# Optimization experiments

Measured on AMD Instinct MI355X. Metric: run time of the kernel, lower is better.

## Reference

```python
import jax, jax.numpy as jnp
import numpy as np

NEG_SLOPE = 0.2
EPS = 1e-12


def setup_inputs() -> dict:
    key = jax.random.key(0)
    ks = jax.random.split(key, 12)
    N, IN, E, C, EF, NET = 100000, 512, 3200000, 16, 64, 8
    return {
        "head_feature": jax.random.normal(ks[0], (N, IN), jnp.float32),
        "tail_feature": jax.random.normal(ks[1], (N, IN), jnp.float32),
        "edge_index": jax.random.randint(ks[2], (2, E), 0, N, jnp.int32),
        "tmp_edge": jax.random.randint(ks[3], (E,), 0, NET, jnp.int32),
        "W": jax.random.normal(ks[4], (IN, C), jnp.float32) * 0.05,
        "W_e": jax.random.normal(ks[5], (EF, EF), jnp.float32) * 0.1,
        "a_l": jax.random.normal(ks[6], (1, 1, C), jnp.float32) * 0.3,
        "a_r": jax.random.normal(ks[7], (1, 1, C), jnp.float32) * 0.3,
        "a_e": jax.random.normal(ks[8], (1, 1, EF), jnp.float32) * 0.3,
        "edge_emb": jax.random.normal(ks[9], (NET, EF), jnp.float32) * 0.3,
        "res_W": jax.random.normal(ks[10], (IN, C), jnp.float32) * 0.05,
        "res_b": jax.random.normal(ks[11], (C,), jnp.float32) * 0.05,
    }


def reference(head_feature, tail_feature, W, W_e, a_l, a_r, a_e,
              edge_emb, res_W, res_b, edge_index, tmp_edge):
    N = head_feature.shape[0]
    H = a_l.shape[1]  # nhead = 1 in SimpleHGN_final's edge_GAT
    C = a_l.shape[2]
    head_ind, tail_ind = edge_index[0], edge_index[1]

    # projected node / edge-type features (dropout is identity in eval)
    h_head = (head_feature @ W).reshape(N, H, C)              # [N,H,C]
    h_tail = (tail_feature @ W).reshape(-1, H, C)             # [Nt,H,C]
    e = (edge_emb @ W_e).reshape(-1, H, a_e.shape[2])         # [NET,H,EF]

    # per-edge attention logits
    h_l = (a_l * h_head).sum(-1)[head_ind]                    # [E,H]
    h_r = (a_r * h_tail).sum(-1)[tail_ind]                    # [E,H]
    h_e = (a_e * e).sum(-1)[tmp_edge]                         # [E,H]
    logits = jax.nn.leaky_relu(h_l + h_r + h_e, NEG_SLOPE)    # [E,H]

    # sparse softmax over each destination (head) row, per head
    m = jax.ops.segment_max(logits, head_ind, num_segments=N)  # [N,H]
    ex = jnp.exp(logits - m[head_ind])
    denom = jax.ops.segment_sum(ex, head_ind, num_segments=N)  # [N,H]
    attn = ex / denom[head_ind]                                # [E,H]

    # SpMM aggregation: out[i] = sum_e attn[e] * h_tail[tail[e]]
    msg = attn[..., None] * h_tail[tail_ind]                   # [E,H,C]
    out = jax.ops.segment_sum(msg, head_ind, num_segments=N)   # [N,H,C]
    out = out.reshape(N, H * C)

    # node residual (nn.Linear on x_head)
    out = out + head_feature @ res_W + res_b

    # SimpleHGN_final post-processing: L2 row-normalize then softmax
    norm = jnp.linalg.norm(out, axis=1, keepdims=True)
    h_prime = out / jnp.maximum(norm, EPS)
    return jax.nn.softmax(h_prime, axis=1)
```

## Files before the change

### kernel.cpp

```cpp
#include <hip/hip_runtime.h>
#include <hip/hip_fp16.h>
#include <math.h>

#define IN_F 512
#define C_DIM 16
#define EF_DIM 64
#define BSHIFT 6
#define NPB 64
#define NBMAX2 2048
#define CNTW 2048
#define SCB 512
#define NSPL 8
#define CAP 2560

typedef float f32x4 __attribute__((ext_vector_type(4)));
typedef _Float16 f16x8 __attribute__((ext_vector_type(8)));

union U2H { unsigned u; __half2 h; };

typedef const unsigned __attribute__((address_space(1)))* gas_u32;
typedef unsigned __attribute__((address_space(3)))* las_u32;

__device__ __forceinline__ void gld16(const float* g, float* l) {
  __builtin_amdgcn_global_load_lds((gas_u32)g, (las_u32)l, 16, 0, 0);
}

__global__ __launch_bounds__(512) void prep_kernel(
    const float* __restrict__ W, const float* __restrict__ We,
    const float* __restrict__ al, const float* __restrict__ ar,
    const float* __restrict__ ae, const float* __restrict__ emb,
    const float* __restrict__ resW, float* __restrict__ he,
    _Float16* __restrict__ Bph, _Float16* __restrict__ Bpt,
    float* __restrict__ wlt, float* __restrict__ wrt, int NET) {
  __shared__ float v[EF_DIM];
  int t = threadIdx.x;
  float wl = 0.f, wr = 0.f;
#pragma unroll
  for (int c = 0; c < C_DIM; c++) {
    float wv = W[t * C_DIM + c];
    wl += wv * al[c];
    wr += wv * ar[c];
  }
  wlt[t] = wl;
  wrt[t] = wr;
  if (t < EF_DIM) {
    float s = 0.f;
    for (int f = 0; f < EF_DIM; f++) s += We[t * EF_DIM + f] * ae[f];
    v[t] = s;
  }
  __syncthreads();
  if (t < NET) {
    float s = 0.f;
    for (int k = 0; k < EF_DIM; k++) s += emb[t * EF_DIM + k] * v[k];
    he[t] = s;
  }
  for (int i = 0; i < 16; i++) {
    int flat = t + 512 * i;
    int j = flat & 7;
    int l = (flat >> 3) & 63;
    int s = flat >> 9;
    int k = 32 * s + ((l >> 4) << 3) + j;
    int c = l & 15;
    Bph[flat] = (_Float16)resW[k * C_DIM + c];
    Bpt[flat] = (_Float16)W[k * C_DIM + c];
  }
}

__global__ __launch_bounds__(256) void projhist_kernel(
    const float* __restrict__ hf, const float* __restrict__ tf,
    const _Float16* __restrict__ Bph, const _Float16* __restrict__ Bpt,
    const float* __restrict__ wlt, const float* __restrict__ wrt,
    float* __restrict__ resid, float* __restrict__ hl,
    __half* __restrict__ ht_, float* __restrict__ hr, int N, int PB,
    const int* __restrict__ head, unsigned* __restrict__ cnt, int E, int NB,
    int chunk) {
  __shared__ __align__(16) float shmem[8192];
  int t = threadIdx.x;
  int bid = blockIdx.x;
  if (bid >= 2 * PB) {
    unsigned* lcnt = (unsigned*)shmem;
    int hb = bid - 2 * PB;
    for (int b = t; b < NB; b += 256) lcnt[b] = 0u;
    __syncthreads();
    int start = hb * chunk;
    int end = min(E, start + chunk);
    for (int i = start + t; i < end; i += 256)
      atomicAdd(
          &lcnt[((unsigned)__builtin_nontemporal_load(head + i)) >> BSHIFT],
          1u);
    __syncthreads();
    unsigned* row = cnt + (size_t)hb * CNTW;
    for (int b = t; b < NB; b += 256) row[b] = lcnt[b];
    return;
  }
  float* As0 = shmem;
  float* As1 = shmem + 4096;
  int w = __builtin_amdgcn_readfirstlane(t >> 6);
  int lane = t & 63;
  int by = bid >= PB ? 1 : 0;
  int r0 = (bid - by * PB) * 64;
  const float* feat = by ? tf : hf;
  const _Float16* Bp = by ? Bpt : Bph;
  const float* wv = by ? wrt : wlt;
  f32x4 acc0 = {0.f, 0.f, 0.f, 0.f};
  float acc1 = 0.f;
  const float* sg_src[4];
#pragma unroll
  for (int g = 0; g < 4; g++) {
    int u = (w * 4 + g) * 64 + lane;
    int r = u >> 4;
    int c = (u & 15) ^ (r & 7);
    int gr = min(r0 + r, N - 1);
    sg_src[g] = feat + (size_t)gr * IN_F + c * 4;
  }
  int row = w * 16 + (lane & 15);
  int sA[2][2];
#pragma unroll
  for (int s2 = 0; s2 < 2; s2++)
#pragma unroll
    for (int h = 0; h < 2; h++)
      sA[s2][h] = row * 16 + ((s2 * 8 + (lane >> 4) * 2 + h) ^ (row & 7));
  const float* wvp = wv + (lane >> 4) * 8;
#pragma unroll
  for (int g = 0; g < 4; g++) gld16(sg_src[g], As0 + (w * 4 + g) * 256);
  __syncthreads();
#pragma unroll
  for (int kc = 0; kc < 8; kc++) {
    if (kc < 7) {
      float* nb = (kc & 1) ? As0 : As1;
#pragma unroll
      for (int g = 0; g < 4; g++)
        gld16(sg_src[g] + (kc + 1) * 64, nb + (w * 4 + g) * 256);
    }
    const float* ab = (kc & 1) ? As1 : As0;
#pragma unroll
    for (int s2 = 0; s2 < 2; s2++) {
      f32x4 lo = *(const f32x4*)(ab + sA[s2][0] * 4);
      f32x4 hi = *(const f32x4*)(ab + sA[s2][1] * 4);
      f16x8 a = {(_Float16)lo.x, (_Float16)lo.y, (_Float16)lo.z,
                 (_Float16)lo.w, (_Float16)hi.x, (_Float16)hi.y,
                 (_Float16)hi.z, (_Float16)hi.w};
      int s = kc * 2 + s2;
      f16x8 b0 = *(const f16x8*)(Bp + (size_t)(s * 64 + lane) * 8);
      acc0 = __builtin_amdgcn_mfma_f32_16x16x32_f16(a, b0, acc0, 0, 0, 0);
      f32x4 wa = *(const f32x4*)(wvp + kc * 64 + s2 * 32);
      f32x4 wb = *(const f32x4*)(wvp + kc * 64 + s2 * 32 + 4);
      acc1 += lo.x * wa.x + lo.y * wa.y + lo.z * wa.z + lo.w * wa.w +
              hi.x * wb.x + hi.y * wb.y + hi.z * wb.z + hi.w * wb.w;
    }
    __syncthreads();
  }
  acc1 += __shfl_xor(acc1, 16, 64);
  acc1 += __shfl_xor(acc1, 32, 64);
  int col = lane & 15;
  int rb = r0 + w * 16 + (lane >> 4) * 4;
#pragma unroll
  for (int i = 0; i < 4; i++) {
    int r = rb + i;
    if (r < N) {
      if (by == 0)
        resid[(size_t)r * C_DIM + col] = acc0[i];
      else
        ht_[(size_t)r * C_DIM + col] = __float2half(acc0[i]);
    }
  }
  if (lane < 16) {
    int r = r0 + w * 16 + lane;
    if (r < N) {
      if (by == 0)
        hl[r] = acc1;
      else
        hr[r] = acc1;
    }
  }
}

__global__ __launch_bounds__(256) void colscanA_kernel(
    unsigned* __restrict__ cnt, unsigned* __restrict__ part, int NB) {
  int b = blockIdx.x * 256 + threadIdx.x;
  if (b >= NB) return;
  int s = blockIdx.y;
  unsigned running = 0;
#pragma unroll 8
  for (int blk = s * 64; blk < s * 64 + 64; blk++) {
    unsigned v = cnt[(size_t)blk * CNTW + b];
    cnt[(size_t)blk * CNTW + b] = running;
    running += v;
  }
  part[(size_t)s * CNTW + b] = running;
}

__global__ __launch_bounds__(256) void colscanB_kernel(
    unsigned* __restrict__ part, unsigned* __restrict__ btotal, int NB) {
  int b = blockIdx.x * 256 + threadIdx.x;
  if (b >= NB) return;
  unsigned running = 0;
#pragma unroll
  for (int s = 0; s < NSPL; s++) {
    unsigned v = part[(size_t)s * CNTW + b];
    part[(size_t)s * CNTW + b] = running;
    running += v;
  }
  btotal[b] = running;
}

__global__ __launch_bounds__(1024) void scan_kernel(
    const unsigned* __restrict__ btotal, unsigned* __restrict__ base, int NB) {
  __shared__ unsigned ps[1024];
  int t = threadIdx.x;
  unsigned a = (2 * t < NB) ? btotal[2 * t] : 0u;
  unsigned b = (2 * t + 1 < NB) ? btotal[2 * t + 1] : 0u;
  ps[t] = a + b;
  __syncthreads();
  for (int off = 1; off < 1024; off <<= 1) {
    unsigned v = (t >= off) ? ps[t - off] : 0u;
    __syncthreads();
    ps[t] += v;
    __syncthreads();
  }
  unsigned excl = ps[t] - (a + b);
  if (2 * t < NB) base[2 * t] = excl;
  if (2 * t + 1 < NB) base[2 * t + 1] = excl + a;
  if (t == 1023) base[NB] = ps[1023];
}

__global__ __launch_bounds__(512) void scatter_kernel(
    const int* __restrict__ head, const int* __restrict__ tail,
    const int* __restrict__ ty, const unsigned* __restrict__ cnt,
    const unsigned* __restrict__ part, const unsigned* __restrict__ bbase,
    unsigned* __restrict__ rec, int E, int NB, int chunk) {
  __shared__ unsigned lbase[NBMAX2];
  __shared__ unsigned lcnt[NBMAX2];
  int tid = threadIdx.x;
  int blk = blockIdx.x;
  const unsigned* row = cnt + (size_t)blk * CNTW;
  const unsigned* prow = part + (size_t)(blk >> 6) * CNTW;
  for (int b = tid; b < NB; b += 512) {
    lbase[b] = bbase[b] + prow[b] + row[b];
    lcnt[b] = 0u;
  }
  __syncthreads();
  int start = blk * chunk;
  int end = min(E, start + chunk);
  for (int i = start + tid; i < end; i += 512) {
    unsigned h = (unsigned)__builtin_nontemporal_load(head + i);
    unsigned tl = (unsigned)__builtin_nontemporal_load(tail + i);
    unsigned t = (unsigned)__builtin_nontemporal_load(ty + i);
    unsigned b = h >> BSHIFT;
    unsigned off = atomicAdd(&lcnt[b], 1u);
    rec[lbase[b] + off] = ((h & 63u) << 20) | ((t & 7u) << 17) | tl;
  }
}

__global__ __launch_bounds__(512) void agg_kernel(
    const unsigned* __restrict__ rec, const unsigned* __restrict__ base,
    const __half* __restrict__ ht, const float* __restrict__ h_l,
    const float* __restrict__ h_r, const float* __restrict__ he_tab,
    const float* __restrict__ resid, const float* __restrict__ resb,
    float* __restrict__ out, int N, int NET) {
  __shared__ unsigned srec[CAP];
  __shared__ unsigned scnt[NPB];
  __shared__ unsigned soff[NPB + 1];
  __shared__ unsigned scur[NPB];
  __shared__ float accf[NPB * 18];
  __shared__ float hl_s[NPB];
  __shared__ float he_s[8];
  int tid = threadIdx.x;
  int b = blockIdx.x;
  int nodebase = b << BSHIFT;
  int s = (int)base[b];
  int e = (int)base[b + 1];
  int cnt_all = e - s;
  int m = min(cnt_all, CAP);
  if (tid < NPB) {
    scnt[tid] = 0u;
    int node = nodebase + tid;
    hl_s[tid] = node < N ? h_l[node] : 0.f;
  }
  if (tid < NET) he_s[tid] = he_tab[tid];
  for (int i = tid; i < NPB * 18; i += 512) accf[i] = 0.f;
  __syncthreads();
  unsigned rv0 = 0, rv1 = 0, rv2 = 0, rv3 = 0, rv4 = 0;
  if (tid < m) rv0 = rec[(size_t)s + tid];
  if (tid + 512 < m) rv1 = rec[(size_t)s + tid + 512];
  if (tid + 1024 < m) rv2 = rec[(size_t)s + tid + 1024];
  if (tid + 1536 < m) rv3 = rec[(size_t)s + tid + 1536];
  if (tid + 2048 < m) rv4 = rec[(size_t)s + tid + 2048];
  if (tid < m) atomicAdd(&scnt[rv0 >> 20], 1u);
  if (tid + 512 < m) atomicAdd(&scnt[rv1 >> 20], 1u);
  if (tid + 1024 < m) atomicAdd(&scnt[rv2 >> 20], 1u);
  if (tid + 1536 < m) atomicAdd(&scnt[rv3 >> 20], 1u);
  if (tid + 2048 < m) atomicAdd(&scnt[rv4 >> 20], 1u);
  __syncthreads();
  if (tid < NPB) {
    unsigned v = scnt[tid];
    unsigned orig = v;
    for (int off = 1; off < NPB; off <<= 1) {
      unsigned u = __shfl_up(v, off, 64);
      if (tid >= off) v += u;
    }
    soff[tid + 1] = v;
    scur[tid] = v - orig;
    if (tid == 0) soff[0] = 0u;
  }
  __syncthreads();
  if (tid < m) srec[atomicAdd(&scur[rv0 >> 20], 1u)] = rv0;
  if (tid + 512 < m) srec[atomicAdd(&scur[rv1 >> 20], 1u)] = rv1;
  if (tid + 1024 < m) srec[atomicAdd(&scur[rv2 >> 20], 1u)] = rv2;
  if (tid + 1536 < m) srec[atomicAdd(&scur[rv3 >> 20], 1u)] = rv3;
  if (tid + 2048 < m) srec[atomicAdd(&scur[rv4 >> 20], 1u)] = rv4;
  for (int i = CAP + tid; i < cnt_all; i += 512) {
    unsigned r = rec[(size_t)(s + i)];
    int local = (int)(r >> 20);
    int typ = (int)((r >> 17) & 7u);
    int tl = (int)(r & 0x1FFFFu);
    float lg = hl_s[local] + h_r[tl] + he_s[typ];
    lg = lg > 0.f ? lg : 0.2f * lg;
    float ex = __expf(lg);
    const uint4* hp = (const uint4*)(ht + (size_t)tl * C_DIM);
    uint4 A = hp[0], B = hp[1];
    float* a = accf + local * 18;
    U2H cv;
    float2 f;
    unsigned wvv[8] = {A.x, A.y, A.z, A.w, B.x, B.y, B.z, B.w};
#pragma unroll
    for (int q = 0; q < 8; q++) {
      cv.u = wvv[q];
      f = __half22float2(cv.h);
      atomicAdd(a + 2 * q, ex * f.x);
      atomicAdd(a + 2 * q + 1, ex * f.y);
    }
    atomicAdd(a + 16, ex);
  }
  __syncthreads();
  int w = tid >> 6;
  int lane = tid & 63;
  int node_l = w * 8 + (lane >> 3);
  int p = lane & 7;
  float a[17];
#pragma unroll
  for (int k = 0; k < 17; k++) a[k] = 0.f;
  int st = (int)soff[node_l];
  int en = (int)soff[node_l + 1];
  float hlv = hl_s[node_l];
  for (int i = st + p; i < en; i += 8) {
    unsigned r = srec[i];
    int typ = (int)((r >> 17) & 7u);
    int tl = (int)(r & 0x1FFFFu);
    float lg = hlv + h_r[tl] + he_s[typ];
    lg = lg > 0.f ? lg : 0.2f * lg;
    float ex = __expf(lg);
    const uint4* hp = (const uint4*)(ht + (size_t)tl * C_DIM);
    uint4 A = hp[0], B = hp[1];
    U2H cv;
    float2 f;
    unsigned wd[8] = {A.x, A.y, A.z, A.w, B.x, B.y, B.z, B.w};
#pragma unroll
    for (int q = 0; q < 8; q++) {
      cv.u = wd[q];
      f = __half22float2(cv.h);
      a[2 * q] += ex * f.x;
      a[2 * q + 1] += ex * f.y;
    }
    a[16] += ex;
  }
#pragma unroll
  for (int k = 0; k < 17; k++) {
    a[k] += __shfl_xor(a[k], 1, 64);
    a[k] += __shfl_xor(a[k], 2, 64);
    a[k] += __shfl_xor(a[k], 4, 64);
  }
  if (p != 0) return;
  int node = nodebase + node_l;
  if (node >= N) return;
  float d = a[16] + accf[node_l * 18 + 16];
  float inv = d > 0.f ? 1.f / d : 0.f;
  const f32x4* r4 = (const f32x4*)(resid + (size_t)node * C_DIM);
  float o[C_DIM];
  float ss = 0.f;
#pragma unroll
  for (int q = 0; q < 4; q++) {
    f32x4 rr = __builtin_nontemporal_load(r4 + q);
    o[4 * q + 0] =
        (a[4 * q + 0] + accf[node_l * 18 + 4 * q + 0]) * inv + rr.x + resb[4 * q + 0];
    o[4 * q + 1] =
        (a[4 * q + 1] + accf[node_l * 18 + 4 * q + 1]) * inv + rr.y + resb[4 * q + 1];
    o[4 * q + 2] =
        (a[4 * q + 2] + accf[node_l * 18 + 4 * q + 2]) * inv + rr.z + resb[4 * q + 2];
    o[4 * q + 3] =
        (a[4 * q + 3] + accf[node_l * 18 + 4 * q + 3]) * inv + rr.w + resb[4 * q + 3];
  }
#pragma unroll
  for (int cc = 0; cc < C_DIM; cc++) ss += o[cc] * o[cc];
  float sc = 1.f / fmaxf(sqrtf(ss), 1e-12f);
  float mx = -1e30f;
#pragma unroll
  for (int cc = 0; cc < C_DIM; cc++) {
    o[cc] *= sc;
    mx = fmaxf(mx, o[cc]);
  }
  float sum = 0.f;
#pragma unroll
  for (int cc = 0; cc < C_DIM; cc++) {
    o[cc] = __expf(o[cc] - mx);
    sum += o[cc];
  }
  float isum = 1.f / sum;
  f32x4* o4 = (f32x4*)(out + (size_t)node * C_DIM);
#pragma unroll
  for (int q = 0; q < 4; q++) {
    f32x4 ov;
    ov.x = o[4 * q] * isum;
    ov.y = o[4 * q + 1] * isum;
    ov.z = o[4 * q + 2] * isum;
    ov.w = o[4 * q + 3] * isum;
    __builtin_nontemporal_store(ov, o4 + q);
  }
}

extern "C" void kernel_launch(void* const* d_in, const int* in_sizes, int n_in,
                              void* d_out, int out_size, void* d_ws,
                              size_t ws_size, hipStream_t stream) {
  const float* head_feature = (const float*)d_in[0];
  const float* tail_feature = (const float*)d_in[1];
  const int* edge_index = (const int*)d_in[2];
  const int* tmp_edge = (const int*)d_in[3];
  const float* W = (const float*)d_in[4];
  const float* We = (const float*)d_in[5];
  const float* al = (const float*)d_in[6];
  const float* ar = (const float*)d_in[7];
  const float* ae = (const float*)d_in[8];
  const float* emb = (const float*)d_in[9];
  const float* resW = (const float*)d_in[10];
  const float* resb = (const float*)d_in[11];

  const int C = in_sizes[6];
  const int IN = in_sizes[4] / C;
  const int N = in_sizes[0] / IN;
  const int E = in_sizes[3];
  const int EF = in_sizes[8];
  const int NET = in_sizes[9] / EF;
  const int NB = (N + NPB - 1) / NPB;
  (void)C; (void)IN; (void)EF; (void)ws_size; (void)out_size; (void)n_in;

  const int* head = edge_index;
  const int* tail = edge_index + E;

  float* ws = (float*)d_ws;
  float* he = ws;
  _Float16* Bph = (_Float16*)(he + 32);
  _Float16* Bpt = Bph + 8192;
  float* wlt = (float*)(Bpt + 8192);
  float* wrt = wlt + 512;
  float* h_l = wrt + 512;
  float* h_r = h_l + N;
  __half* ht = (__half*)(h_r + N);
  float* resid = (float*)(ht + (size_t)C_DIM * N);
  unsigned* rec = (unsigned*)(resid + (size_t)C_DIM * N);
  unsigned* cnt = rec + (size_t)E;
  unsigned* part = cnt + (size_t)SCB * CNTW;
  unsigned* btotal = part + (size_t)NSPL * CNTW;
  unsigned* bbase = btotal + NBMAX2;

  prep_kernel<<<1, 512, 0, stream>>>(W, We, al, ar, ae, emb, resW, he, Bph,
                                     Bpt, wlt, wrt, NET);
  int PB = (N + 63) / 64;
  int chunk = (E + SCB - 1) / SCB;
  projhist_kernel<<<2 * PB + SCB, 256, 0, stream>>>(
      head_feature, tail_feature, Bph, Bpt, wlt, wrt, resid, h_l, ht, h_r, N,
      PB, head, cnt, E, NB, chunk);
  dim3 cg((NB + 255) / 256, NSPL);
  colscanA_kernel<<<cg, 256, 0, stream>>>(cnt, part, NB);
  colscanB_kernel<<<(NB + 255) / 256, 256, 0, stream>>>(part, btotal, NB);
  scan_kernel<<<1, 1024, 0, stream>>>(btotal, bbase, NB);
  scatter_kernel<<<SCB, 512, 0, stream>>>(head, tail, tmp_edge, cnt, part,
                                          bbase, rec, E, NB, chunk);
  agg_kernel<<<NB, 512, 0, stream>>>(rec, bbase, ht, h_l, h_r, he, resid,
                                     resb, (float*)d_out, N, NET);
}
```

Measured before the change: 225.2 us.

## Regroup kernels: fuse histogram into prep, scatter into projection

Moves the per-block head histogram into the single-block prep kernel launch, and merges the edge scatter pass with the node projection GEMM kernel, which now runs after the scans. This removes one kernel launch and lets the memory-bound scatter overlap with the compute-heavier projection blocks. The trade-off is that the histogram no longer overlaps the projection, and the scatter now runs with 256-thread blocks instead of 512.

Result: faster. 201.3 us (-10.6%).

```diff
diff --git a/kernel.cpp b/kernel.cpp
--- a/kernel.cpp
+++ b/kernel.cpp
@@ -25,15 +25,33 @@
   __builtin_amdgcn_global_load_lds((gas_u32)g, (las_u32)l, 16, 0, 0);
 }
 
-__global__ __launch_bounds__(512) void prep_kernel(
+__global__ __launch_bounds__(512) void prephist_kernel(
     const float* __restrict__ W, const float* __restrict__ We,
     const float* __restrict__ al, const float* __restrict__ ar,
     const float* __restrict__ ae, const float* __restrict__ emb,
     const float* __restrict__ resW, float* __restrict__ he,
     _Float16* __restrict__ Bph, _Float16* __restrict__ Bpt,
-    float* __restrict__ wlt, float* __restrict__ wrt, int NET) {
+    float* __restrict__ wlt, float* __restrict__ wrt, int NET,
+    const int* __restrict__ head, unsigned* __restrict__ cnt, int E, int NB,
+    int chunk) {
+  __shared__ unsigned lcnt[NBMAX2];
   __shared__ float v[EF_DIM];
   int t = threadIdx.x;
+  int bid = blockIdx.x;
+  if (bid < SCB) {
+    for (int b = t; b < NB; b += 512) lcnt[b] = 0u;
+    __syncthreads();
+    int start = bid * chunk;
+    int end = min(E, start + chunk);
+    for (int i = start + t; i < end; i += 512)
+      atomicAdd(
+          &lcnt[((unsigned)__builtin_nontemporal_load(head + i)) >> BSHIFT],
+          1u);
+    __syncthreads();
+    unsigned* row = cnt + (size_t)bid * CNTW;
+    for (int b = t; b < NB; b += 512) row[b] = lcnt[b];
+    return;
+  }
   float wl = 0.f, wr = 0.f;
 #pragma unroll
   for (int c = 0; c < C_DIM; c++) {
@@ -66,39 +84,48 @@
   }
 }
 
-__global__ __launch_bounds__(256) void projhist_kernel(
+__global__ __launch_bounds__(256) void projscatter_kernel(
     const float* __restrict__ hf, const float* __restrict__ tf,
     const _Float16* __restrict__ Bph, const _Float16* __restrict__ Bpt,
     const float* __restrict__ wlt, const float* __restrict__ wrt,
     float* __restrict__ resid, float* __restrict__ hl,
     __half* __restrict__ ht_, float* __restrict__ hr, int N, int PB,
-    const int* __restrict__ head, unsigned* __restrict__ cnt, int E, int NB,
-    int chunk) {
+    const int* __restrict__ head, const int* __restrict__ tail,
+    const int* __restrict__ ty, const unsigned* __restrict__ cnt,
+    const unsigned* __restrict__ part, const unsigned* __restrict__ bbase,
+    unsigned* __restrict__ rec, int E, int NB, int chunk) {
   __shared__ __align__(16) float shmem[8192];
   int t = threadIdx.x;
   int bid = blockIdx.x;
-  if (bid >= 2 * PB) {
-    unsigned* lcnt = (unsigned*)shmem;
-    int hb = bid - 2 * PB;
-    for (int b = t; b < NB; b += 256) lcnt[b] = 0u;
-    __syncthreads();
-    int start = hb * chunk;
+  if (bid < SCB) {
+    unsigned* lbase = (unsigned*)shmem;
+    unsigned* lcnt = lbase + NBMAX2;
+    const unsigned* row = cnt + (size_t)bid * CNTW;
+    const unsigned* prow = part + (size_t)(bid >> 6) * CNTW;
+    for (int b = t; b < NB; b += 256) {
+      lbase[b] = bbase[b] + prow[b] + row[b];
+      lcnt[b] = 0u;
+    }
+    __syncthreads();
+    int start = bid * chunk;
     int end = min(E, start + chunk);
-    for (int i = start + t; i < end; i += 256)
-      atomicAdd(
-          &lcnt[((unsigned)__builtin_nontemporal_load(head + i)) >> BSHIFT],
-          1u);
-    __syncthreads();
-    unsigned* row = cnt + (size_t)hb * CNTW;
-    for (int b = t; b < NB; b += 256) row[b] = lcnt[b];
+    for (int i = start + t; i < end; i += 256) {
+      unsigned h = (unsigned)__builtin_nontemporal_load(head + i);
+      unsigned tl = (unsigned)__builtin_nontemporal_load(tail + i);
+      unsigned tt = (unsigned)__builtin_nontemporal_load(ty + i);
+      unsigned b = h >> BSHIFT;
+      unsigned off = atomicAdd(&lcnt[b], 1u);
+      rec[lbase[b] + off] = ((h & 63u) << 20) | ((tt & 7u) << 17) | tl;
+    }
     return;
   }
   float* As0 = shmem;
   float* As1 = shmem + 4096;
   int w = __builtin_amdgcn_readfirstlane(t >> 6);
   int lane = t & 63;
-  int by = bid >= PB ? 1 : 0;
-  int r0 = (bid - by * PB) * 64;
+  int pbid = bid - SCB;
+  int by = pbid >= PB ? 1 : 0;
+  int r0 = (pbid - by * PB) * 64;
   const float* feat = by ? tf : hf;
   const _Float16* Bp = by ? Bpt : Bph;
   const float* wv = by ? wrt : wlt;
@@ -222,34 +249,6 @@
   if (2 * t < NB) base[2 * t] = excl;
   if (2 * t + 1 < NB) base[2 * t + 1] = excl + a;
   if (t == 1023) base[NB] = ps[1023];
-}
-
-__global__ __launch_bounds__(512) void scatter_kernel(
-    const int* __restrict__ head, const int* __restrict__ tail,
-    const int* __restrict__ ty, const unsigned* __restrict__ cnt,
-    const unsigned* __restrict__ part, const unsigned* __restrict__ bbase,
-    unsigned* __restrict__ rec, int E, int NB, int chunk) {
-  __shared__ unsigned lbase[NBMAX2];
-  __shared__ unsigned lcnt[NBMAX2];
-  int tid = threadIdx.x;
-  int blk = blockIdx.x;
-  const unsigned* row = cnt + (size_t)blk * CNTW;
-  const unsigned* prow = part + (size_t)(blk >> 6) * CNTW;
-  for (int b = tid; b < NB; b += 512) {
-    lbase[b] = bbase[b] + prow[b] + row[b];
-    lcnt[b] = 0u;
-  }
-  __syncthreads();
-  int start = blk * chunk;
-  int end = min(E, start + chunk);
-  for (int i = start + tid; i < end; i += 512) {
-    unsigned h = (unsigned)__builtin_nontemporal_load(head + i);
-    unsigned tl = (unsigned)__builtin_nontemporal_load(tail + i);
-    unsigned t = (unsigned)__builtin_nontemporal_load(ty + i);
-    unsigned b = h >> BSHIFT;
-    unsigned off = atomicAdd(&lcnt[b], 1u);
-    rec[lbase[b] + off] = ((h & 63u) << 20) | ((t & 7u) << 17) | tl;
-  }
 }
 
 __global__ __launch_bounds__(512) void agg_kernel(
@@ -462,19 +461,18 @@
   unsigned* btotal = part + (size_t)NSPL * CNTW;
   unsigned* bbase = btotal + NBMAX2;
 
-  prep_kernel<<<1, 512, 0, stream>>>(W, We, al, ar, ae, emb, resW, he, Bph,
-                                     Bpt, wlt, wrt, NET);
   int PB = (N + 63) / 64;
   int chunk = (E + SCB - 1) / SCB;
-  projhist_kernel<<<2 * PB + SCB, 256, 0, stream>>>(
-      head_feature, tail_feature, Bph, Bpt, wlt, wrt, resid, h_l, ht, h_r, N,
-      PB, head, cnt, E, NB, chunk);
+  prephist_kernel<<<SCB + 1, 512, 0, stream>>>(W, We, al, ar, ae, emb, resW,
+                                               he, Bph, Bpt, wlt, wrt, NET,
+                                               head, cnt, E, NB, chunk);
   dim3 cg((NB + 255) / 256, NSPL);
   colscanA_kernel<<<cg, 256, 0, stream>>>(cnt, part, NB);
   colscanB_kernel<<<(NB + 255) / 256, 256, 0, stream>>>(part, btotal, NB);
   scan_kernel<<<1, 1024, 0, stream>>>(btotal, bbase, NB);
-  scatter_kernel<<<SCB, 512, 0, stream>>>(head, tail, tmp_edge, cnt, part,
-                                          bbase, rec, E, NB, chunk);
+  projscatter_kernel<<<SCB + 2 * PB, 256, 0, stream>>>(
+      head_feature, tail_feature, Bph, Bpt, wlt, wrt, resid, h_l, ht, h_r, N,
+      PB, head, tail, tmp_edge, cnt, part, bbase, rec, E, NB, chunk);
   agg_kernel<<<NB, 512, 0, stream>>>(rec, bbase, ht, h_l, h_r, he, resid,
                                      resb, (float*)d_out, N, NET);
 }
```
